# Optimization experiments

Measured on AMD Instinct MI355X. Metric: run time of the kernel, lower is better.

The kernel has to match this reference:

```python
import jax, jax.numpy as jnp
import numpy as np


def setup_inputs() -> dict:
    key = jax.random.key(0)
    ks = jax.random.split(key, 8)
    B, S, D, N = 16, 1024, 128, 128
    s = lambda fan: 1.0 / np.sqrt(fan)
    return {
        "x": jax.random.normal(ks[0], (B, S, D), jnp.float32),
        "umask": jax.random.randint(ks[1], (B, S), 0, 2, jnp.int32),
        # proj_n: Mlp over sequence axis (in=S, hidden=out=N)
        "w_n1": jax.random.normal(ks[2], (S, N), jnp.float32) * s(S),
        "b_n1": jnp.zeros((N,), jnp.float32),
        "w_n2": jax.random.normal(ks[3], (N, N), jnp.float32) * s(N),
        "b_n2": jnp.zeros((N,), jnp.float32),
        # proj_d: Mlp over feature axis (in=D_e, hidden=out=prompt_dim)
        "w_d1": jax.random.normal(ks[4], (D, D), jnp.float32) * s(D),
        "b_d1": jnp.zeros((D,), jnp.float32),
        "w_d2": jax.random.normal(ks[5], (D, D), jnp.float32) * s(D),
        "b_d2": jnp.zeros((D,), jnp.float32),
        # proj_prompt: Linear(D_e -> prompt_dim)
        "w_p": jax.random.normal(ks[6], (D, D), jnp.float32) * s(D),
        "b_p": jnp.zeros((D,), jnp.float32),
    }


def reference(x, umask, w_n1, b_n1, w_n2, b_n2, w_d1, b_d1, w_d2, b_d2, w_p, b_p):
    B, S, D = x.shape
    # proj_n over the sequence axis: x^T is [B, D, S] -> [B, D, N]
    xt = jnp.swapaxes(x, 1, 2)
    proto = jax.nn.gelu(xt @ w_n1 + b_n1, approximate=False) @ w_n2 + b_n2
    proto = jnp.swapaxes(proto, 1, 2).reshape(-1, D)  # [B*N, D]
    # cosine similarity over flattened batch: [B*S, B*N]
    xf = x.reshape(-1, D)
    xn = xf / jnp.linalg.norm(xf, axis=1, keepdims=True)
    pn = proto / jnp.linalg.norm(proto, axis=1, keepdims=True)
    sim = xn @ pn.T
    # per-row mask (broadcast instead of the original wasteful repeat)
    mask = (1.0 - umask.reshape(-1).astype(x.dtype))[:, None] * -10000.0
    attn = jax.nn.softmax(sim + mask, axis=1)
    prompt = (attn @ proto).reshape(B, S, D)
    prompt = jax.nn.gelu(prompt @ w_d1 + b_d1, approximate=False) @ w_d2 + b_d2
    res = x @ w_p + b_p
    return (prompt + res, proto, res)
```

## Files before the change

### kernel.cpp

```cpp
#include <hip/hip_runtime.h>
#include <math.h>

#define B_ 16
#define S_ 1024
#define D_ 128
#define N_ 128
#define BS_ (B_*S_)
#define BN_ (B_*N_)
#define LOG2E 1.442695040888963f

typedef __attribute__((ext_vector_type(8))) short short8b;
typedef __attribute__((ext_vector_type(4))) float f32x4;
typedef __attribute__((ext_vector_type(4))) unsigned short us4;
typedef __attribute__((ext_vector_type(4))) unsigned int u32x4;

__device__ __forceinline__ float gelu_exact(float x) {
    return 0.5f * x * (1.0f + erff(x * 0.70710678118654752440f));
}

__device__ __forceinline__ unsigned short f2bf(float f) {
    unsigned u = __builtin_bit_cast(unsigned, f);
    unsigned r = (u + 0x7FFFu + ((u >> 16) & 1u)) >> 16;
    return (unsigned short)r;
}
__device__ __forceinline__ unsigned int pk2(float lo, float hi) {
    return (unsigned)f2bf(lo) | ((unsigned)f2bf(hi) << 16);
}

__device__ __forceinline__ void gl16(const void* g, void* l) {
    __builtin_amdgcn_global_load_lds((const __attribute__((address_space(1))) unsigned int*)g,
                                     (__attribute__((address_space(3))) unsigned int*)l,
                                     16, 0, 0);
}


__global__ __launch_bounds__(256) void k0a_xprep(const float* __restrict__ x,
                                                 unsigned short* __restrict__ xnbf,
                                                 unsigned short* __restrict__ xT,
                                                 float* __restrict__ xnorm) {
    __shared__ __align__(16) unsigned int T2[128 * 32];
    const int b  = blockIdx.x >> 4;
    const int s0 = (blockIdx.x & 15) * 64;
    const int t  = threadIdx.x;
    const int rp = t >> 3;
    const int q  = t & 7;
    const int row0 = s0 + 2 * rp;
    const float* p0 = x + ((size_t)b * S_ + row0) * D_ + q * 16;
    const float* p1 = p0 + D_;
    f32x4 a[4], c[4];
    #pragma unroll
    for (int i = 0; i < 4; ++i) { a[i] = ((const f32x4*)p0)[i]; c[i] = ((const f32x4*)p1)[i]; }
    float sa = 0.f, sc = 0.f;
    #pragma unroll
    for (int i = 0; i < 4; ++i)
        #pragma unroll
        for (int j = 0; j < 4; ++j) { sa += a[i][j]*a[i][j]; sc += c[i][j]*c[i][j]; }
    sa += __shfl_xor(sa, 1); sa += __shfl_xor(sa, 2); sa += __shfl_xor(sa, 4);
    sc += __shfl_xor(sc, 1); sc += __shfl_xor(sc, 2); sc += __shfl_xor(sc, 4);
    const float na = sqrtf(sa), nc = sqrtf(sc);
    if (q == 0) {
        xnorm[(size_t)b*S_ + row0]     = na;
        xnorm[(size_t)b*S_ + row0 + 1] = nc;
    }
    const float ia = 1.0f / na, ic = 1.0f / nc;
    unsigned int pk[8];
    #pragma unroll
    for (int i = 0; i < 4; ++i) {
        pk[2*i]   = pk2(a[i][0]*ia, a[i][1]*ia);
        pk[2*i+1] = pk2(a[i][2]*ia, a[i][3]*ia);
    }
    *(u32x4*)(xnbf + ((size_t)b*S_ + row0)*D_ + q*16)     = *(u32x4*)&pk[0];
    *(u32x4*)(xnbf + ((size_t)b*S_ + row0)*D_ + q*16 + 8) = *(u32x4*)&pk[4];
    #pragma unroll
    for (int i = 0; i < 4; ++i) {
        pk[2*i]   = pk2(c[i][0]*ic, c[i][1]*ic);
        pk[2*i+1] = pk2(c[i][2]*ic, c[i][3]*ic);
    }
    *(u32x4*)(xnbf + ((size_t)b*S_ + row0 + 1)*D_ + q*16)     = *(u32x4*)&pk[0];
    *(u32x4*)(xnbf + ((size_t)b*S_ + row0 + 1)*D_ + q*16 + 8) = *(u32x4*)&pk[4];
    #pragma unroll
    for (int i = 0; i < 4; ++i)
        #pragma unroll
        for (int j = 0; j < 4; ++j) {
            const int d = q*16 + i*4 + j;
            *(unsigned int*)((char*)T2 + d*128 + ((rp*4) ^ (((d>>3)&7)<<4))) =
                pk2(a[i][j], c[i][j]);
        }
    __syncthreads();
    const int d  = t >> 1;
    const int hf = t & 1;
    unsigned short* dst = xT + ((size_t)(b*128 + d))*1024 + s0 + hf*32;
    #pragma unroll
    for (int cI = 0; cI < 4; ++cI) {
        const int sp0 = hf*16 + cI*4;
        u32x4 v = *(u32x4*)((char*)T2 + d*128 + ((sp0*4) ^ (((d>>3)&7)<<4)));
        *(u32x4*)(dst + cI*8) = v;
    }
}

__global__ __launch_bounds__(256) void k0b_wprep(const float* __restrict__ w1,
                                                 const float* __restrict__ w2,
                                                 const float* __restrict__ wp,
                                                 const float* __restrict__ wd1,
                                                 const float* __restrict__ wd2,
                                                 unsigned short* __restrict__ w1T,
                                                 unsigned short* __restrict__ w2T,
                                                 unsigned short* __restrict__ wpT,
                                                 unsigned short* __restrict__ wd1T,
                                                 unsigned short* __restrict__ wd2T) {
    __shared__ __align__(16) unsigned int T2[64 * 32];
    const int bi = blockIdx.x;
    const float* src; unsigned short* dst; int R, r0, c0;
    if (bi < 32) {
        src = w1; dst = w1T; R = 1024;
        r0 = (bi >> 1) * 64; c0 = (bi & 1) * 64;
    } else {
        const int k = (bi - 32) >> 2, qd = (bi - 32) & 3;
        const float* ss[4] = {w2, wp, wd1, wd2};
        unsigned short* dd[4] = {w2T, wpT, wd1T, wd2T};
        src = ss[k]; dst = dd[k]; R = 128;
        r0 = (qd >> 1) * 64; c0 = (qd & 1) * 64;
    }
    const int t = threadIdx.x;
    const int rp = t >> 3, q = t & 7;
    const float* p0 = src + (size_t)(r0 + 2*rp) * 128 + c0 + q*8;
    const float* p1 = p0 + 128;
    f32x4 a0 = ((const f32x4*)p0)[0], a1 = ((const f32x4*)p0)[1];
    f32x4 b0 = ((const f32x4*)p1)[0], b1 = ((const f32x4*)p1)[1];
    #pragma unroll
    for (int j = 0; j < 4; ++j) {
        int cc = q*8 + j;
        *(unsigned int*)((char*)T2 + cc*128 + ((rp*4) ^ (((cc>>3)&7)<<4))) = pk2(a0[j], b0[j]);
        cc = q*8 + 4 + j;
        *(unsigned int*)((char*)T2 + cc*128 + ((rp*4) ^ (((cc>>3)&7)<<4))) = pk2(a1[j], b1[j]);
    }
    __syncthreads();
    const int cI = t >> 2, qt = t & 3;
    unsigned short* od = dst + (size_t)(c0 + cI) * R + r0 + qt*16;
    #pragma unroll
    for (int u = 0; u < 2; ++u) {
        const int sp0 = qt*8 + u*4;
        u32x4 v = *(u32x4*)((char*)T2 + cI*128 + ((sp0*4) ^ (((cI>>3)&7)<<4)));
        *(u32x4*)(od + u*8) = v;
    }
}

__global__ __launch_bounds__(512) void k12_proto(const unsigned short* __restrict__ xT,
                                                 const unsigned short* __restrict__ w1T,
                                                 const float* __restrict__ b_n1,
                                                 const unsigned short* __restrict__ w2T,
                                                 const float* __restrict__ b_n2,
                                                 float* __restrict__ out1,
                                                 unsigned short* __restrict__ pbf,
                                                 unsigned short* __restrict__ pbfT) {
    __shared__ __align__(16) unsigned short pool[2][2][128 * 64];
    __shared__ __align__(16) unsigned short GT[128][136];
    __shared__ float nrm[128][2];
    const int b = blockIdx.x;
    const int tid = threadIdx.x;
    const int w = tid >> 6, l = tid & 63, l15 = l & 15, lh = l >> 4;
    const int mb = (w & 3) * 32;
    const int db = (w >> 2) * 64;

    f32x4 acc[2][4] = {};

    #define STAGE_A(buf, itt)                                                        \
        { _Pragma("unroll")                                                          \
          for (int i = 0; i < 2; ++i) {                                              \
            const int s = tid + 512*i;                                               \
            const int r = s >> 3, chs = s & 7;                                       \
            gl16(w1T + (size_t)r*1024 + (itt)*64 + (chs ^ (r & 7))*8,                \
                 &pool[buf][0][s*8]);                                                \
            gl16(xT + ((size_t)(b*128 + r))*1024 + (itt)*64 + (chs ^ (r & 7))*8,     \
                 &pool[buf][1][s*8]);                                                \
          } }

    STAGE_A(0, 0)
    asm volatile("s_waitcnt vmcnt(0)");
    __syncthreads();
    int cur = 0;
    for (int it = 0; it < 16; ++it) {
        if (it < 15) {
            STAGE_A(cur ^ 1, it + 1)
        } else {
            #pragma unroll
            for (int i = 0; i < 4; ++i) {
                const int s = tid + 512*i;
                const int r = s >> 4, chs = s & 15;
                gl16(w2T + (size_t)r*128 + (chs ^ (r & 7))*8,
                     ((unsigned short*)pool[0]) + s*8);
            }
        }
        const unsigned short* WA = pool[cur][0];
        const unsigned short* XA = pool[cur][1];
        #pragma unroll
        for (int kc = 0; kc < 2; ++kc) {
            short8b Af[2], Bf[4];
            #pragma unroll
            for (int mt = 0; mt < 2; ++mt) {
                const int m = mb + mt*16 + l15;
                Af[mt] = *(const short8b*)(WA + m*64 + ((kc*4 + lh) ^ (m & 7))*8);
            }
            #pragma unroll
            for (int dt = 0; dt < 4; ++dt) {
                const int d = db + dt*16 + l15;
                Bf[dt] = *(const short8b*)(XA + d*64 + ((kc*4 + lh) ^ (d & 7))*8);
            }
            #pragma unroll
            for (int mt = 0; mt < 2; ++mt)
                #pragma unroll
                for (int dt = 0; dt < 4; ++dt)
                    acc[mt][dt] = __builtin_amdgcn_mfma_f32_16x16x32_bf16(Af[mt], Bf[dt], acc[mt][dt], 0, 0, 0);
        }
        asm volatile("s_waitcnt vmcnt(0)");
        __syncthreads();
        cur ^= 1;
    }
    #pragma unroll
    for (int mt = 0; mt < 2; ++mt)
        #pragma unroll
        for (int dt = 0; dt < 4; ++dt)
            #pragma unroll
            for (int u = 0; u < 2; ++u) {
                const int m = mb + mt*16 + lh*4 + 2*u;
                const int d = db + dt*16 + l15;
                const float v0 = gelu_exact(acc[mt][dt][2*u]   + b_n1[m]);
                const float v1 = gelu_exact(acc[mt][dt][2*u+1] + b_n1[m+1]);
                *(unsigned int*)((char*)&GT[0][0] + d*272 + m*2) = pk2(v0, v1);
            }
    __syncthreads();
    const unsigned short* W2 = (const unsigned short*)pool[0];
    f32x4 acc2[2][4] = {};
    #pragma unroll
    for (int kc = 0; kc < 4; ++kc) {
        short8b Af[2], Bf[4];
        #pragma unroll
        for (int nt = 0; nt < 2; ++nt) {
            const int n = mb + nt*16 + l15;
            Af[nt] = *(const short8b*)(W2 + n*128 + ((kc*4 + lh) ^ (n & 7))*8);
        }
        #pragma unroll
        for (int dt = 0; dt < 4; ++dt) {
            const int d = db + dt*16 + l15;
            Bf[dt] = *(const short8b*)((char*)&GT[0][0] + d*272 + kc*64 + lh*16);
        }
        #pragma unroll
        for (int nt = 0; nt < 2; ++nt)
            #pragma unroll
            for (int dt = 0; dt < 4; ++dt)
                acc2[nt][dt] = __builtin_amdgcn_mfma_f32_16x16x32_bf16(Af[nt], Bf[dt], acc2[nt][dt], 0, 0, 0);
    }
    #pragma unroll
    for (int nt = 0; nt < 2; ++nt) {
        #pragma unroll
        for (int jr = 0; jr < 4; ++jr) {
            const int n = mb + nt*16 + lh*4 + jr;
            const float bb = b_n2[n];
            float ps = 0.f;
            #pragma unroll
            for (int dt = 0; dt < 4; ++dt) {
                const int d = db + dt*16 + l15;
                const float v = acc2[nt][dt][jr] + bb;
                acc2[nt][dt][jr] = v;
                out1[((size_t)(b*128 + n))*128 + d] = v;
                ps += v * v;
            }
            ps += __shfl_xor(ps, 1); ps += __shfl_xor(ps, 2);
            ps += __shfl_xor(ps, 4); ps += __shfl_xor(ps, 8);
            if (l15 == 0) nrm[n][w >> 2] = ps;
        }
    }
    __syncthreads();
    unsigned short* TP = (unsigned short*)pool[1];
    #pragma unroll
    for (int nt = 0; nt < 2; ++nt)
        #pragma unroll
        for (int jr = 0; jr < 4; ++jr) {
            const int n = mb + nt*16 + lh*4 + jr;
            const float pin = 1.0f / sqrtf(nrm[n][0] + nrm[n][1]);
            #pragma unroll
            for (int dt = 0; dt < 4; ++dt) {
                const int d = db + dt*16 + l15;
                pbf[((size_t)(b*128 + n))*128 + d] = f2bf(acc2[nt][dt][jr] * pin);
            }
        }
    #pragma unroll
    for (int nt = 0; nt < 2; ++nt)
        #pragma unroll
        for (int dt = 0; dt < 4; ++dt)
            #pragma unroll
            for (int u = 0; u < 2; ++u) {
                const int n0 = mb + nt*16 + lh*4 + 2*u;
                const int d = db + dt*16 + l15;
                *(unsigned int*)((char*)TP + d*256 + ((n0*2) ^ ((d & 7) << 4))) =
                    pk2(acc2[nt][dt][2*u], acc2[nt][dt][2*u+1]);
            }
    __syncthreads();
    if (tid < 256) {
        const int d = tid >> 1, hf = tid & 1;
        #pragma unroll
        for (int cI = 0; cI < 8; ++cI) {
            short8b v = *(const short8b*)((char*)TP + d*256 + ((hf*128 + cI*16) ^ ((d & 7) << 4)));
            *(short8b*)(pbfT + (size_t)d*BN_ + b*128 + hf*64 + cI*8) = v;
        }
    }
}

__global__ __launch_bounds__(256) void k4_attn_mfma(const unsigned short* __restrict__ xnbf,
                                                    const unsigned short* __restrict__ pbf,
                                                    const unsigned short* __restrict__ pbfT,
                                                    unsigned short* __restrict__ pbm) {
    __shared__ __align__(16) unsigned short K_lds[2][2][64 * 128];
    __shared__ __align__(16) unsigned short V_lds[2][2][128 * 64];
    __shared__ __align__(16) unsigned short P_lds[4][32 * 64];
    const int tid = threadIdx.x;
    const int w = tid >> 6, l = tid & 63, l15 = l & 15, lh = l >> 4;
    const int qg = w & 1, kh = w >> 1;
    const int q0 = blockIdx.x * 64;
    const int qb = q0 + qg * 32;
    short8b Xf[2][4];
    #pragma unroll
    for (int g = 0; g < 2; ++g)
        #pragma unroll
        for (int kk = 0; kk < 4; ++kk)
            Xf[g][kk] = *(const short8b*)(xnbf + (size_t)(qb + g*16 + l15)*D_ + kk*32 + lh*8);

    const int half = tid >> 7;
    const int ht = tid & 127;

    #define STAGE_KV(buf, itt)                                                       \
        { const int t0s = half * 1024 + (itt) * 64;                                  \
          unsigned short* KB_ = K_lds[half][buf];                                    \
          unsigned short* VB_ = V_lds[half][buf];                                    \
          _Pragma("unroll")                                                          \
          for (int i = 0; i < 8; ++i) {                                              \
            const int s = ht + 128*i;                                                \
            { const int key = s >> 4, chs = s & 15;                                  \
              gl16(pbf + (size_t)(t0s + key)*128 + (chs ^ (key & 7))*8, KB_ + s*8); }\
            { const int d = s >> 3, c2 = s & 7;                                      \
              gl16(pbfT + (size_t)d*BN_ + t0s + (c2 ^ (d & 7))*8, VB_ + s*8); }      \
          } }

    STAGE_KV(0, 0)
    float lsum[2] = {0.f, 0.f};
    f32x4 acc[2][8] = {};
    asm volatile("s_waitcnt vmcnt(0)");
    __syncthreads();
    int cur = 0;
    for (int it = 0; it < 16; ++it) {
        if (it < 15) STAGE_KV(cur ^ 1, it + 1)
        const unsigned short* KB = K_lds[kh][cur];
        const unsigned short* VB = V_lds[kh][cur];
        f32x4 S[2][4] = {};
        #pragma unroll
        for (int kk = 0; kk < 4; ++kk) {
            #pragma unroll
            for (int kt = 0; kt < 4; ++kt) {
                const int key = kt*16 + l15;
                short8b Kf = *(const short8b*)(KB + key*128 + ((kk*4 + lh) ^ (key & 7))*8);
                S[0][kt] = __builtin_amdgcn_mfma_f32_16x16x32_bf16(Kf, Xf[0][kk], S[0][kt], 0, 0, 0);
                S[1][kt] = __builtin_amdgcn_mfma_f32_16x16x32_bf16(Kf, Xf[1][kk], S[1][kt], 0, 0, 0);
            }
        }
        unsigned short* PW = P_lds[w];
        #pragma unroll
        for (int g = 0; g < 2; ++g)
            #pragma unroll
            for (int kt = 0; kt < 4; ++kt) {
                us4 pk;
                #pragma unroll
                for (int jr = 0; jr < 4; ++jr) {
                    const float p = exp2f((S[g][kt][jr] - 1.0f) * LOG2E);
                    lsum[g] += p;
                    pk[jr] = f2bf(p);
                }
                const int chunk = (kt*2 + (lh >> 1)) ^ (l15 & 7);
                *(us4*)&PW[(g*16 + l15)*64 + chunk*8 + (lh & 1)*4] = pk;
            }
        short8b Pf[2][2];
        #pragma unroll
        for (int g = 0; g < 2; ++g)
            #pragma unroll
            for (int kkk = 0; kkk < 2; ++kkk)
                Pf[g][kkk] = *(const short8b*)&PW[(g*16 + l15)*64 + ((kkk*4 + lh) ^ (l15 & 7))*8];
        #pragma unroll
        for (int nb = 0; nb < 8; ++nb) {
            const int d = nb*16 + l15;
            short8b Vf0 = *(const short8b*)(VB + d*64 + ((lh)     ^ (d & 7))*8);
            short8b Vf1 = *(const short8b*)(VB + d*64 + ((4 + lh) ^ (d & 7))*8);
            acc[0][nb] = __builtin_amdgcn_mfma_f32_16x16x32_bf16(Pf[0][0], Vf0, acc[0][nb], 0, 0, 0);
            acc[0][nb] = __builtin_amdgcn_mfma_f32_16x16x32_bf16(Pf[0][1], Vf1, acc[0][nb], 0, 0, 0);
            acc[1][nb] = __builtin_amdgcn_mfma_f32_16x16x32_bf16(Pf[1][0], Vf0, acc[1][nb], 0, 0, 0);
            acc[1][nb] = __builtin_amdgcn_mfma_f32_16x16x32_bf16(Pf[1][1], Vf1, acc[1][nb], 0, 0, 0);
        }
        asm volatile("s_waitcnt vmcnt(0)");
        __syncthreads();
        cur ^= 1;
    }
    #pragma unroll
    for (int g = 0; g < 2; ++g) {
        lsum[g] += __shfl_xor(lsum[g], 16);
        lsum[g] += __shfl_xor(lsum[g], 32);
    }
    float* Obuf = (float*)&K_lds[0][0][0];
    float* lbuf = (float*)&V_lds[0][0][0];
    if (kh == 1) {
        #pragma unroll
        for (int g = 0; g < 2; ++g)
            #pragma unroll
            for (int nb = 0; nb < 8; ++nb)
                #pragma unroll
                for (int jr = 0; jr < 4; ++jr) {
                    const int row = qg*32 + g*16 + lh*4 + jr;
                    Obuf[row*132 + nb*16 + l15] = acc[g][nb][jr];
                }
        if (l < 16) { lbuf[qg*32 + l15] = lsum[0]; lbuf[qg*32 + 16 + l15] = lsum[1]; }
    }
    __syncthreads();
    if (kh == 0) {
        #pragma unroll
        for (int g = 0; g < 2; ++g) {
            const float inv = 1.0f / (lsum[g] + lbuf[qg*32 + g*16 + l15]);
            #pragma unroll
            for (int jr = 0; jr < 4; ++jr) {
                const float rl = __shfl(inv, lh*4 + jr, 64);
                #pragma unroll
                for (int nb = 0; nb < 8; ++nb) {
                    const int row = qg*32 + g*16 + lh*4 + jr;
                    const float o = (acc[g][nb][jr] + Obuf[row*132 + nb*16 + l15]) * rl;
                    pbm[(size_t)(q0 + row)*D_ + nb*16 + l15] = f2bf(o);
                }
            }
        }
    }
}

__global__ __launch_bounds__(256) void k_res_mfma(const unsigned short* __restrict__ xnbf,
                                                  const float* __restrict__ xnorm,
                                                  const unsigned short* __restrict__ wpT,
                                                  const float* __restrict__ bp,
                                                  float* __restrict__ out2) {
    __shared__ __align__(16) unsigned short XA[64 * 128];
    __shared__ __align__(16) unsigned short WB[128 * 128];
    const int tid = threadIdx.x;
    const int w = tid >> 6, l = tid & 63, l15 = l & 15, lh = l >> 4;
    const int r0 = blockIdx.x * 64;
    #pragma unroll
    for (int i = 0; i < 4; ++i) {
        const int s = tid + 256*i;
        const int r = s >> 4, chs = s & 15;
        gl16(xnbf + (size_t)(r0 + r)*128 + (chs ^ (r & 7))*8, XA + s*8);
    }
    #pragma unroll
    for (int i = 0; i < 8; ++i) {
        const int s = tid + 256*i;
        const int r = s >> 4, chs = s & 15;
        gl16(wpT + (size_t)r*128 + (chs ^ (r & 7))*8, WB + s*8);
    }
    asm volatile("s_waitcnt vmcnt(0)");
    __syncthreads();
    const int rb = w * 16;
    f32x4 acc[8] = {};
    #pragma unroll
    for (int kc = 0; kc < 4; ++kc) {
        const int r = rb + l15;
        short8b Af = *(const short8b*)(XA + r*128 + ((kc*4 + lh) ^ (r & 7))*8);
        #pragma unroll
        for (int cb = 0; cb < 8; ++cb) {
            const int c = cb*16 + l15;
            short8b Bf = *(const short8b*)(WB + c*128 + ((kc*4 + lh) ^ (c & 7))*8);
            acc[cb] = __builtin_amdgcn_mfma_f32_16x16x32_bf16(Af, Bf, acc[cb], 0, 0, 0);
        }
    }
    #pragma unroll
    for (int jr = 0; jr < 4; ++jr) {
        const int r = r0 + rb + lh*4 + jr;
        const float xn = xnorm[r];
        #pragma unroll
        for (int cb = 0; cb < 8; ++cb) {
            const int c = cb*16 + l15;
            out2[(size_t)r*128 + c] = xn * acc[cb][jr] + bp[c];
        }
    }
}

__global__ __launch_bounds__(256) void k5_mlp_mfma(const unsigned short* __restrict__ pbm,
                                                   const unsigned short* __restrict__ wd1T,
                                                   const float* __restrict__ b1,
                                                   const unsigned short* __restrict__ wd2T,
                                                   const float* __restrict__ b2,
                                                   const float* __restrict__ res,
                                                   float* __restrict__ out0) {
    __shared__ __align__(16) unsigned short PA[64 * 128];
    __shared__ __align__(16) unsigned short W1B[128 * 128];
    __shared__ __align__(16) unsigned short W2B[128 * 128];
    __shared__ __align__(16) unsigned short T1[64 * 128];
    const int tid = threadIdx.x;
    const int w = tid >> 6, l = tid & 63, l15 = l & 15, lh = l >> 4;
    const int r0 = blockIdx.x * 64;
    #pragma unroll
    for (int i = 0; i < 4; ++i) {
        const int s = tid + 256*i;
        const int r = s >> 4, chs = s & 15;
        gl16(pbm + (size_t)(r0 + r)*128 + (chs ^ (r & 7))*8, PA + s*8);
    }
    #pragma unroll
    for (int i = 0; i < 8; ++i) {
        const int s = tid + 256*i;
        const int r = s >> 4, chs = s & 15;
        gl16(wd1T + (size_t)r*128 + (chs ^ (r & 7))*8, W1B + s*8);
        gl16(wd2T + (size_t)r*128 + (chs ^ (r & 7))*8, W2B + s*8);
    }
    asm volatile("s_waitcnt vmcnt(0)");
    __syncthreads();
    const int rb = w * 16;
    f32x4 acc1[8] = {};
    #pragma unroll
    for (int kc = 0; kc < 4; ++kc) {
        const int r = rb + l15;
        short8b Af = *(const short8b*)(PA + r*128 + ((kc*4 + lh) ^ (r & 7))*8);
        #pragma unroll
        for (int hb = 0; hb < 8; ++hb) {
            const int h = hb*16 + l15;
            short8b Bf = *(const short8b*)(W1B + h*128 + ((kc*4 + lh) ^ (h & 7))*8);
            acc1[hb] = __builtin_amdgcn_mfma_f32_16x16x32_bf16(Af, Bf, acc1[hb], 0, 0, 0);
        }
    }
    #pragma unroll
    for (int hb = 0; hb < 8; ++hb) {
        const int h = hb*16 + l15;
        const float bb = b1[h];
        #pragma unroll
        for (int jr = 0; jr < 4; ++jr) {
            const int r = rb + lh*4 + jr;
            const float v = gelu_exact(acc1[hb][jr] + bb);
            *(unsigned short*)((char*)T1 + r*256 + ((h*2) ^ ((r & 7) << 4))) = f2bf(v);
        }
    }
    __syncthreads();
    f32x4 acc2[8] = {};
    #pragma unroll
    for (int kc = 0; kc < 4; ++kc) {
        const int r = rb + l15;
        short8b Af = *(const short8b*)((char*)T1 + r*256 + ((kc*64 + lh*16) ^ ((r & 7) << 4)));
        #pragma unroll
        for (int cb = 0; cb < 8; ++cb) {
            const int c = cb*16 + l15;
            short8b Bf = *(const short8b*)(W2B + c*128 + ((kc*4 + lh) ^ (c & 7))*8);
            acc2[cb] = __builtin_amdgcn_mfma_f32_16x16x32_bf16(Af, Bf, acc2[cb], 0, 0, 0);
        }
    }
    #pragma unroll
    for (int cb = 0; cb < 8; ++cb) {
        const int c = cb*16 + l15;
        const float bb = b2[c];
        #pragma unroll
        for (int jr = 0; jr < 4; ++jr) {
            const int r = r0 + rb + lh*4 + jr;
            out0[(size_t)r*128 + c] = acc2[cb][jr] + bb + res[(size_t)r*128 + c];
        }
    }
}

extern "C" void kernel_launch(void* const* d_in, const int* in_sizes, int n_in,
                              void* d_out, int out_size, void* d_ws, size_t ws_size,
                              hipStream_t stream) {
    const float* x    = (const float*)d_in[0];
    const float* w_n1 = (const float*)d_in[2];
    const float* b_n1 = (const float*)d_in[3];
    const float* w_n2 = (const float*)d_in[4];
    const float* b_n2 = (const float*)d_in[5];
    const float* w_d1 = (const float*)d_in[6];
    const float* b_d1 = (const float*)d_in[7];
    const float* w_d2 = (const float*)d_in[8];
    const float* b_d2 = (const float*)d_in[9];
    const float* w_p  = (const float*)d_in[10];
    const float* b_p  = (const float*)d_in[11];

    float* out0 = (float*)d_out;
    float* out1 = out0 + (size_t)BS_ * D_;
    float* out2 = out1 + (size_t)BN_ * D_;

    char* ws = (char*)d_ws;
    unsigned short* xnbf = (unsigned short*)ws;
    unsigned short* xT   = (unsigned short*)(ws + (4u << 20));
    unsigned short* pbm  = xT;
    float* xnorm         = (float*)(ws + (8u << 20));
    unsigned short* w1T  = (unsigned short*)(ws + (8u << 20) + (64u << 10));
    unsigned short* w2T  = w1T + 128 * 1024;
    unsigned short* wpT  = w2T + 128 * 128;
    unsigned short* wd1T = wpT + 128 * 128;
    unsigned short* wd2T = wd1T + 128 * 128;
    unsigned short* pbf  = wd2T + 128 * 128;
    unsigned short* pbfT = pbf + (size_t)BN_ * D_;

    hipLaunchKernelGGL(k0a_xprep,   dim3(256), dim3(256), 0, stream, x, xnbf, xT, xnorm);
    hipLaunchKernelGGL(k0b_wprep,   dim3(48),  dim3(256), 0, stream, w_n1, w_n2, w_p, w_d1, w_d2,
                       w1T, w2T, wpT, wd1T, wd2T);
    hipLaunchKernelGGL(k12_proto,   dim3(16),  dim3(512), 0, stream, xT, w1T, b_n1, w2T, b_n2,
                       out1, pbf, pbfT);
    hipLaunchKernelGGL(k_res_mfma,  dim3(256), dim3(256), 0, stream, xnbf, xnorm, wpT, b_p, out2);
    hipLaunchKernelGGL(k4_attn_mfma,dim3(256), dim3(256), 0, stream, xnbf, pbf, pbfT, pbm);
    hipLaunchKernelGGL(k5_mlp_mfma, dim3(256), dim3(256), 0, stream, pbm, wd1T, b_d1, wd2T, b_d2,
                       out2, out0);
}
```

Measured before the change: 177.1 us.

## Split attention keys across blocks with 32x32 MFMA and separate combine kernel

```diff
diff --git a/kernel.cpp b/kernel.cpp
--- a/kernel.cpp
+++ b/kernel.cpp
@@ -11,6 +11,7 @@
 
 typedef __attribute__((ext_vector_type(8))) short short8b;
 typedef __attribute__((ext_vector_type(4))) float f32x4;
+typedef __attribute__((ext_vector_type(16))) float f32x16;
 typedef __attribute__((ext_vector_type(4))) unsigned short us4;
 typedef __attribute__((ext_vector_type(4))) unsigned int u32x4;
 
@@ -306,133 +307,137 @@
     }
 }
 
-__global__ __launch_bounds__(256) void k4_attn_mfma(const unsigned short* __restrict__ xnbf,
-                                                    const unsigned short* __restrict__ pbf,
-                                                    const unsigned short* __restrict__ pbfT,
-                                                    unsigned short* __restrict__ pbm) {
-    __shared__ __align__(16) unsigned short K_lds[2][2][64 * 128];
-    __shared__ __align__(16) unsigned short V_lds[2][2][128 * 64];
-    __shared__ __align__(16) unsigned short P_lds[4][32 * 64];
+__global__ __launch_bounds__(256, 2) void k4a_attn(const unsigned short* __restrict__ xnbf,
+                                                   const unsigned short* __restrict__ pbf,
+                                                   const unsigned short* __restrict__ pbfT,
+                                                   float* __restrict__ Op0,
+                                                   float* __restrict__ Op1,
+                                                   float* __restrict__ lpart) {
+    __shared__ __align__(16) unsigned short Kb[2][64 * 128];
+    __shared__ __align__(16) unsigned short Vb[2][128 * 64];
     const int tid = threadIdx.x;
-    const int w = tid >> 6, l = tid & 63, l15 = l & 15, lh = l >> 4;
-    const int qg = w & 1, kh = w >> 1;
-    const int q0 = blockIdx.x * 64;
-    const int qb = q0 + qg * 32;
-    short8b Xf[2][4];
-    #pragma unroll
-    for (int g = 0; g < 2; ++g)
-        #pragma unroll
-        for (int kk = 0; kk < 4; ++kk)
-            Xf[g][kk] = *(const short8b*)(xnbf + (size_t)(qb + g*16 + l15)*D_ + kk*32 + lh*8);
-
-    const int half = tid >> 7;
-    const int ht = tid & 127;
-
-    #define STAGE_KV(buf, itt)                                                       \
-        { const int t0s = half * 1024 + (itt) * 64;                                  \
-          unsigned short* KB_ = K_lds[half][buf];                                    \
-          unsigned short* VB_ = V_lds[half][buf];                                    \
-          _Pragma("unroll")                                                          \
-          for (int i = 0; i < 8; ++i) {                                              \
-            const int s = ht + 128*i;                                                \
-            { const int key = s >> 4, chs = s & 15;                                  \
-              gl16(pbf + (size_t)(t0s + key)*128 + (chs ^ (key & 7))*8, KB_ + s*8); }\
-            { const int d = s >> 3, c2 = s & 7;                                      \
-              gl16(pbfT + (size_t)d*BN_ + t0s + (c2 ^ (d & 7))*8, VB_ + s*8); }      \
-          } }
-
-    STAGE_KV(0, 0)
-    float lsum[2] = {0.f, 0.f};
-    f32x4 acc[2][8] = {};
-    asm volatile("s_waitcnt vmcnt(0)");
-    __syncthreads();
-    int cur = 0;
-    for (int it = 0; it < 16; ++it) {
-        if (it < 15) STAGE_KV(cur ^ 1, it + 1)
-        const unsigned short* KB = K_lds[kh][cur];
-        const unsigned short* VB = V_lds[kh][cur];
-        f32x4 S[2][4] = {};
-        #pragma unroll
-        for (int kk = 0; kk < 4; ++kk) {
-            #pragma unroll
-            for (int kt = 0; kt < 4; ++kt) {
-                const int key = kt*16 + l15;
-                short8b Kf = *(const short8b*)(KB + key*128 + ((kk*4 + lh) ^ (key & 7))*8);
-                S[0][kt] = __builtin_amdgcn_mfma_f32_16x16x32_bf16(Kf, Xf[0][kk], S[0][kt], 0, 0, 0);
-                S[1][kt] = __builtin_amdgcn_mfma_f32_16x16x32_bf16(Kf, Xf[1][kk], S[1][kt], 0, 0, 0);
-            }
-        }
-        unsigned short* PW = P_lds[w];
-        #pragma unroll
-        for (int g = 0; g < 2; ++g)
-            #pragma unroll
-            for (int kt = 0; kt < 4; ++kt) {
-                us4 pk;
+    const int w = tid >> 6, l = tid & 63;
+    const int l31 = l & 31, hi = l >> 5;
+    const int qg = w & 1, kq = w >> 1;
+    const int qblk = blockIdx.x >> 1, half = blockIdx.x & 1;
+    const int qb = qblk * 64 + qg * 32;
+    float* __restrict__ Opart = half ? Op1 : Op0;
+
+    short8b Xf[8];
+    #pragma unroll
+    for (int kc = 0; kc < 8; ++kc)
+        Xf[kc] = *(const short8b*)(xnbf + (size_t)(qb + l31) * D_ + kc * 16 + hi * 8);
+
+    f32x16 acc[4] = {};
+    float lsum = 0.f;
+
+    #define STG(buf, g)  {                                                    \
+        const int t0s = half * 1024 + (g) * 64;                               \
+        _Pragma("unroll")                                                     \
+        for (int i = 0; i < 4; ++i) {                                         \
+            const int sK = tid + 256 * i;                                     \
+            const int rK = sK >> 4, cK = (sK & 15) ^ (rK & 15);               \
+            gl16(pbf + (size_t)(t0s + rK) * D_ + cK * 8, Kb[buf] + sK * 8);   \
+            const int dV = sK >> 3, cV = (sK & 7) ^ (dV & 7);                 \
+            gl16(pbfT + (size_t)dV * BN_ + t0s + cV * 8, Vb[buf] + sK * 8);   \
+        } }
+
+    STG(0, 0)
+    __syncthreads();
+    for (int g = 0; g < 16; ++g) {
+        if (g < 15) STG((g + 1) & 1, g + 1)
+        if (kq == (g & 1)) {
+            const unsigned short* KB = Kb[g & 1];
+            const unsigned short* VB = Vb[g & 1];
+            f32x16 S[2] = {};
+            #pragma unroll
+            for (int kc = 0; kc < 8; ++kc) {
+                const int cs = ((kc * 2 + hi) ^ (l31 & 15)) * 8;
+                short8b K0 = *(const short8b*)(KB + l31 * 128 + cs);
+                short8b K1 = *(const short8b*)(KB + (32 + l31) * 128 + cs);
+                S[0] = __builtin_amdgcn_mfma_f32_32x32x16_bf16(K0, Xf[kc], S[0], 0, 0, 0);
+                S[1] = __builtin_amdgcn_mfma_f32_32x32x16_bf16(K1, Xf[kc], S[1], 0, 0, 0);
+            }
+            short8b Pf[4];
+            #pragma unroll
+            for (int kt = 0; kt < 2; ++kt) {
+                float p[16];
                 #pragma unroll
-                for (int jr = 0; jr < 4; ++jr) {
-                    const float p = exp2f((S[g][kt][jr] - 1.0f) * LOG2E);
-                    lsum[g] += p;
-                    pk[jr] = f2bf(p);
+                for (int r = 0; r < 16; ++r) {
+                    p[r] = exp2f((S[kt][r] - 1.0f) * LOG2E);
+                    lsum += p[r];
                 }
-                const int chunk = (kt*2 + (lh >> 1)) ^ (l15 & 7);
-                *(us4*)&PW[(g*16 + l15)*64 + chunk*8 + (lh & 1)*4] = pk;
-            }
-        short8b Pf[2][2];
-        #pragma unroll
-        for (int g = 0; g < 2; ++g)
-            #pragma unroll
-            for (int kkk = 0; kkk < 2; ++kkk)
-                Pf[g][kkk] = *(const short8b*)&PW[(g*16 + l15)*64 + ((kkk*4 + lh) ^ (l15 & 7))*8];
-        #pragma unroll
-        for (int nb = 0; nb < 8; ++nb) {
-            const int d = nb*16 + l15;
-            short8b Vf0 = *(const short8b*)(VB + d*64 + ((lh)     ^ (d & 7))*8);
-            short8b Vf1 = *(const short8b*)(VB + d*64 + ((4 + lh) ^ (d & 7))*8);
-            acc[0][nb] = __builtin_amdgcn_mfma_f32_16x16x32_bf16(Pf[0][0], Vf0, acc[0][nb], 0, 0, 0);
-            acc[0][nb] = __builtin_amdgcn_mfma_f32_16x16x32_bf16(Pf[0][1], Vf1, acc[0][nb], 0, 0, 0);
-            acc[1][nb] = __builtin_amdgcn_mfma_f32_16x16x32_bf16(Pf[1][0], Vf0, acc[1][nb], 0, 0, 0);
-            acc[1][nb] = __builtin_amdgcn_mfma_f32_16x16x32_bf16(Pf[1][1], Vf1, acc[1][nb], 0, 0, 0);
-        }
-        asm volatile("s_waitcnt vmcnt(0)");
+                #pragma unroll
+                for (int h = 0; h < 2; ++h) {
+                    unsigned int wA0 = pk2(p[8*h+0], p[8*h+1]);
+                    unsigned int wA1 = pk2(p[8*h+2], p[8*h+3]);
+                    unsigned int wB0 = pk2(p[8*h+4], p[8*h+5]);
+                    unsigned int wB1 = pk2(p[8*h+6], p[8*h+7]);
+                    asm("v_permlane32_swap_b32 %0, %1" : "+v"(wB0), "+v"(wA0));
+                    asm("v_permlane32_swap_b32 %0, %1" : "+v"(wB1), "+v"(wA1));
+                    u32x4 pw; pw[0] = wA0; pw[1] = wA1; pw[2] = wB0; pw[3] = wB1;
+                    Pf[kt*2 + h] = __builtin_bit_cast(short8b, pw);
+                }
+            }
+            #pragma unroll
+            for (int kc2 = 0; kc2 < 4; ++kc2) {
+                #pragma unroll
+                for (int dt = 0; dt < 4; ++dt) {
+                    const int d = dt * 32 + l31;
+                    short8b Vf = *(const short8b*)(VB + d * 64 + (((kc2*2+hi) ^ (d & 7)) * 8));
+                    acc[dt] = __builtin_amdgcn_mfma_f32_32x32x16_bf16(Pf[kc2], Vf, acc[dt], 0, 0, 0);
+                }
+            }
+        }
         __syncthreads();
-        cur ^= 1;
-    }
-    #pragma unroll
-    for (int g = 0; g < 2; ++g) {
-        lsum[g] += __shfl_xor(lsum[g], 16);
-        lsum[g] += __shfl_xor(lsum[g], 32);
-    }
-    float* Obuf = (float*)&K_lds[0][0][0];
-    float* lbuf = (float*)&V_lds[0][0][0];
-    if (kh == 1) {
-        #pragma unroll
-        for (int g = 0; g < 2; ++g)
-            #pragma unroll
-            for (int nb = 0; nb < 8; ++nb)
-                #pragma unroll
-                for (int jr = 0; jr < 4; ++jr) {
-                    const int row = qg*32 + g*16 + lh*4 + jr;
-                    Obuf[row*132 + nb*16 + l15] = acc[g][nb][jr];
-                }
-        if (l < 16) { lbuf[qg*32 + l15] = lsum[0]; lbuf[qg*32 + 16 + l15] = lsum[1]; }
-    }
-    __syncthreads();
-    if (kh == 0) {
-        #pragma unroll
-        for (int g = 0; g < 2; ++g) {
-            const float inv = 1.0f / (lsum[g] + lbuf[qg*32 + g*16 + l15]);
-            #pragma unroll
-            for (int jr = 0; jr < 4; ++jr) {
-                const float rl = __shfl(inv, lh*4 + jr, 64);
-                #pragma unroll
-                for (int nb = 0; nb < 8; ++nb) {
-                    const int row = qg*32 + g*16 + lh*4 + jr;
-                    const float o = (acc[g][nb][jr] + Obuf[row*132 + nb*16 + l15]) * rl;
-                    pbm[(size_t)(q0 + row)*D_ + nb*16 + l15] = f2bf(o);
-                }
-            }
-        }
-    }
+    }
+    lsum += __shfl_xor(lsum, 32);
+
+    float* Obuf = (float*)&Kb[0][0];
+    float* lbuf = (float*)&Vb[0][0];
+    if (kq == 0) {
+        #pragma unroll
+        for (int dt = 0; dt < 4; ++dt)
+            #pragma unroll
+            for (int r = 0; r < 16; ++r) {
+                const int qr = (r & 3) + 8 * (r >> 2) + 4 * hi;
+                Obuf[qg * 4096 + qr * 128 + dt * 32 + l31] = acc[dt][r];
+            }
+        if (!hi) lbuf[qg * 32 + l31] = lsum;
+    }
+    __syncthreads();
+    if (kq == 1) {
+        #pragma unroll
+        for (int dt = 0; dt < 4; ++dt)
+            #pragma unroll
+            for (int r = 0; r < 16; ++r) {
+                const int qr = (r & 3) + 8 * (r >> 2) + 4 * hi;
+                const float v = acc[dt][r] + Obuf[qg * 4096 + qr * 128 + dt * 32 + l31];
+                Opart[(size_t)(qb + qr) * D_ + dt * 32 + l31] = v;
+            }
+        if (!hi) lpart[half * BS_ + qb + l31] = lsum + lbuf[qg * 32 + l31];
+    }
+}
+
+__global__ __launch_bounds__(256) void k4b_comb(const float* __restrict__ Op0,
+                                                const float* __restrict__ Op1,
+                                                const float* __restrict__ lpart,
+                                                unsigned short* __restrict__ pbm) {
+    const int t = blockIdx.x * 256 + threadIdx.x;
+    const int row = t >> 3, d0 = (t & 7) * 16;
+    const float inv = 1.0f / (lpart[row] + lpart[BS_ + row]);
+    const float* a = Op0 + (size_t)row * D_ + d0;
+    const float* b = Op1 + (size_t)row * D_ + d0;
+    unsigned int wo[8];
+    #pragma unroll
+    for (int i = 0; i < 4; ++i) {
+        f32x4 va = ((const f32x4*)a)[i];
+        f32x4 vb = ((const f32x4*)b)[i];
+        wo[2*i]   = pk2((va[0]+vb[0])*inv, (va[1]+vb[1])*inv);
+        wo[2*i+1] = pk2((va[2]+vb[2])*inv, (va[3]+vb[3])*inv);
+    }
+    *(u32x4*)(pbm + (size_t)row * D_ + d0)     = *(u32x4*)&wo[0];
+    *(u32x4*)(pbm + (size_t)row * D_ + d0 + 8) = *(u32x4*)&wo[4];
 }
 
 __global__ __launch_bounds__(256) void k_res_mfma(const unsigned short* __restrict__ xnbf,
@@ -593,6 +598,9 @@
     unsigned short* wd2T = wd1T + 128 * 128;
     unsigned short* pbf  = wd2T + 128 * 128;
     unsigned short* pbfT = pbf + (size_t)BN_ * D_;
+    float* Opart0        = out0;
+    float* Opart1        = (float*)(ws + (10u << 20));
+    float* lpart         = (float*)(ws + (18u << 20));
 
     hipLaunchKernelGGL(k0a_xprep,   dim3(256), dim3(256), 0, stream, x, xnbf, xT, xnorm);
     hipLaunchKernelGGL(k0b_wprep,   dim3(48),  dim3(256), 0, stream, w_n1, w_n2, w_p, w_d1, w_d2,
@@ -600,7 +608,9 @@
     hipLaunchKernelGGL(k12_proto,   dim3(16),  dim3(512), 0, stream, xT, w1T, b_n1, w2T, b_n2,
                        out1, pbf, pbfT);
     hipLaunchKernelGGL(k_res_mfma,  dim3(256), dim3(256), 0, stream, xnbf, xnorm, wpT, b_p, out2);
-    hipLaunchKernelGGL(k4_attn_mfma,dim3(256), dim3(256), 0, stream, xnbf, pbf, pbfT, pbm);
+    hipLaunchKernelGGL(k4a_attn,    dim3(512), dim3(256), 0, stream, xnbf, pbf, pbfT,
+                       Opart0, Opart1, lpart);
+    hipLaunchKernelGGL(k4b_comb,    dim3(512), dim3(256), 0, stream, Opart0, Opart1, lpart, pbm);
     hipLaunchKernelGGL(k5_mlp_mfma, dim3(256), dim3(256), 0, stream, pbm, wd1T, b_d1, wd2T, b_d2,
                        out2, out0);
 }
```

Measured after the change: 177.1 us. Within noise of the previous version (-0.0%).
